# Kernel optimization log

Measured on AMD Instinct MI355X. Metric: run time of the kernel, lower is better.

Reference implementation:

```python
import jax, jax.numpy as jnp
import numpy as np

OFFSET = 1.0
BANDWIDTH = 0.5
EPS = 1e-5


def _similarity(source, target):
    # source: [b, c, h, w] -> [b, ns, c]; target: [b, c, h2, w2] -> [b, nt, c]
    b, c = source.shape[0], source.shape[1]
    s = source.reshape(b, c, -1).transpose(0, 2, 1)                  # [b, ns, c]
    t = target.reshape(b, target.shape[1], -1).transpose(0, 2, 1)    # [b, nt, c]
    s_sqr = jnp.sum(s * s, axis=-1)                                  # [b, ns]
    t_sqr = jnp.sum(t * t, axis=-1)                                  # [b, nt]
    # pairwise squared distances [b, nt, ns]
    dist = t_sqr[:, :, None] - 2.0 * jnp.einsum('btc,bsc->bts', t, s) + s_sqr[:, None, :]
    dist = jnp.maximum(dist, 0.0)
    # per source-column min over target rows (chunking in torch is per-column, hence equivalent globally)
    min_dist = jnp.min(dist, axis=1, keepdims=True)                  # [b, 1, ns]
    sim = jnp.exp((OFFSET - dist / (min_dist + EPS)) / BANDWIDTH)    # [b, nt, ns]
    sim = sim / jnp.sum(sim, axis=1, keepdims=True)                  # column-normalize over target dim
    # max over source columns per target row, then mean over target rows
    return jnp.mean(jnp.max(sim, axis=2), axis=-1)                   # [b]


def _loss(source, target):
    return jnp.mean(-jnp.log(_similarity(source, target)))


def setup_inputs() -> dict:
    key = jax.random.key(0)
    k1, k2 = jax.random.split(key)
    source = jax.random.normal(k1, (2, 128, 64, 64), dtype=jnp.float32)
    target = jax.random.normal(k2, (2, 128, 64, 64), dtype=jnp.float32)
    return {"source": source, "target": target}


def reference(source, target):
    # is_symmetric=True, is_similarity=False -> symmetric loss
    return (_loss(source, target) + _loss(target, source)) / 2.0
```

## Files before the change

kernel.cpp:

```cpp
#include <hip/hip_runtime.h>
#include <math.h>

#define NB 2
#define NC 128
#define NN 4096
#define C2L 2.88539008177792681472f

typedef __attribute__((ext_vector_type(8))) short short8;
typedef __attribute__((ext_vector_type(4))) float f32x4;

__device__ unsigned short g_Tb[NB][NN][NC];
__device__ unsigned short g_Sb[NB][NN][NC];
__device__ float g_tsqr[NB][NN];
__device__ float g_ssqr[NB][NN];
__device__ float g_rowS[NB][NN];
__device__ float g_rowLZ[NB][NN];
__device__ float g_rowE[NB][NN];
__device__ float g_colS[NB][NN];
__device__ float g_colLZ[NB][NN];
__device__ float g_colE[NB][NN];
__device__ float g_colpart[NB][128][NN];
__device__ float g_rowpart[NB][16][NN];

#if __has_builtin(__builtin_amdgcn_exp2f)
__device__ __forceinline__ float fexp2(float x) { return __builtin_amdgcn_exp2f(x); }
#else
__device__ __forceinline__ float fexp2(float x) { return exp2f(x); }
#endif

#define GLL16(gsrc, ldst) \
  __builtin_amdgcn_global_load_lds((const __attribute__((address_space(1))) void*)(gsrc), \
                                   (__attribute__((address_space(3))) void*)(ldst), 16, 0, 0)

__device__ __forceinline__ unsigned f2bf(float f) {
    unsigned u = __float_as_uint(f);
    u += 0x7FFFu + ((u >> 16) & 1u);
    return u >> 16;
}

__global__ void __launch_bounds__(256) transpose_prep(const float* __restrict__ src,
                                                      const float* __restrict__ tgt) {
    __shared__ float ls[NC][68];
    __shared__ float redn[4][64];
    int bid = blockIdx.x;
    int mat = bid >> 7;
    int b   = (bid >> 6) & 1;
    int n0  = (bid & 63) << 6;
    int tid = threadIdx.x;
    const float* in = (mat ? tgt : src) + (size_t)b * NC * NN;
    unsigned short (*out)[NC] = mat ? g_Tb[b] : g_Sb[b];
    float* sq = mat ? g_tsqr[b] : g_ssqr[b];

    for (int idx = tid; idx < NC * 16; idx += 256) {
        int k = idx >> 4, c4 = (idx & 15) << 2;
        *(float4*)&ls[k][c4] = *(const float4*)(in + (size_t)k * NN + n0 + c4);
    }
    __syncthreads();
    {
        int n = tid & 63, c = tid >> 6;
        float psum = 0.f;
        for (int cc = c; cc < 16; cc += 4) {
            unsigned uo[4];
            #pragma unroll
            for (int e = 0; e < 4; ++e) {
                float v0 = ls[cc * 8 + 2 * e][n];
                float v1 = ls[cc * 8 + 2 * e + 1][n];
                psum = fmaf(v0, v0, psum);
                psum = fmaf(v1, v1, psum);
                uo[e] = f2bf(v0) | (f2bf(v1) << 16);
            }
            int swz = mat ? cc : (cc ^ (n & 7));
            *(uint4*)&out[n0 + n][swz * 8] = make_uint4(uo[0], uo[1], uo[2], uo[3]);
        }
        redn[c][n] = psum;
    }
    __syncthreads();
    if (tid < 64)
        sq[n0 + tid] = (redn[0][tid] + redn[1][tid]) + (redn[2][tid] + redn[3][tid]);
}

template<int PASS>
__global__ void __launch_bounds__(256) sweep_kernel() {
    __shared__ unsigned short Sp[256 * NC];

    int bid = blockIdx.x;
    int b   = bid >> 9;
    int st  = (bid >> 4) & 31;
    int pn  = bid & 15;
    int i0  = st * 128;
    int j0  = pn * 256;
    int tid = threadIdx.x;
    int w = tid >> 6, lane = tid & 63, q = lane >> 4, x = lane & 15;
    int iw = i0 + w * 32;

    #pragma unroll
    for (int it = 0; it < 16; ++it) {
        int l = tid + it * 256;
        GLL16(&g_Sb[b][j0 + (l >> 4)][(l & 15) * 8], &Sp[l * 8]);
    }

    short8 af[2][4];
    #pragma unroll
    for (int m = 0; m < 2; ++m)
        #pragma unroll
        for (int kk = 0; kk < 4; ++kk)
            af[m][kk] = *(const short8*)&g_Tb[b][iw + m * 16 + x][(kk * 4 + q) * 8];

    float tq[8], rS[8], rC[8];
    #pragma unroll
    for (int m = 0; m < 2; ++m)
        #pragma unroll
        for (int v = 0; v < 4; ++v) {
            int row = iw + m * 16 + q * 4 + v;
            tq[m * 4 + v] = g_tsqr[b][row];
            rS[m * 4 + v] = (PASS >= 2) ? g_rowS[b][row] : 0.f;
            rC[m * 4 + v] = (PASS == 3) ? (C2L - g_rowLZ[b][row]) : 0.f;
        }

    float sqc[4], cSc[4], cCc[4], sqn[4], cSn[4], cCn[4];
    #pragma unroll
    for (int n = 0; n < 4; ++n) {
        int col = j0 + n * 16 + x;
        sqn[n] = g_ssqr[b][col];
        cSn[n] = (PASS >= 2) ? g_colS[b][col] : 0.f;
        cCn[n] = (PASS == 3) ? (C2L - g_colLZ[b][col]) : 0.f;
    }

    float rstate[8];
    #pragma unroll
    for (int e = 0; e < 8; ++e)
        rstate[e] = (PASS == 1) ? 3.0e38f : (PASS == 2 ? 0.f : -3.0e38f);

    __syncthreads();

    for (int jt = 0; jt < 4; ++jt) {
        #pragma unroll
        for (int n = 0; n < 4; ++n) { sqc[n] = sqn[n]; cSc[n] = cSn[n]; cCc[n] = cCn[n]; }
        if (jt < 3) {
            #pragma unroll
            for (int n = 0; n < 4; ++n) {
                int col = j0 + (jt + 1) * 64 + n * 16 + x;
                sqn[n] = g_ssqr[b][col];
                if (PASS >= 2) cSn[n] = g_colS[b][col];
                if (PASS == 3) cCn[n] = C2L - g_colLZ[b][col];
            }
        }

        f32x4 acc[2][4];
        #pragma unroll
        for (int m = 0; m < 2; ++m)
            #pragma unroll
            for (int n = 0; n < 4; ++n)
                acc[m][n] = (f32x4){0.f, 0.f, 0.f, 0.f};

        #pragma unroll
        for (int kk = 0; kk < 4; ++kk) {
            short8 bf[4];
            #pragma unroll
            for (int n = 0; n < 4; ++n) {
                int r  = jt * 64 + n * 16 + x;
                int ch = (kk * 4 + q) ^ (r & 7);
                bf[n] = *(const short8*)&Sp[r * NC + ch * 8];
            }
            #pragma unroll
            for (int m = 0; m < 2; ++m)
                #pragma unroll
                for (int n = 0; n < 4; ++n)
                    acc[m][n] = __builtin_amdgcn_mfma_f32_16x16x32_bf16(af[m][kk], bf[n], acc[m][n], 0, 0, 0);
        }

        float cstate[4];
        #pragma unroll
        for (int n = 0; n < 4; ++n)
            cstate[n] = (PASS == 1) ? 3.0e38f : (PASS == 2 ? 0.f : -3.0e38f);

        #pragma unroll
        for (int m = 0; m < 2; ++m)
            #pragma unroll
            for (int n = 0; n < 4; ++n)
                #pragma unroll
                for (int v = 0; v < 4; ++v) {
                    float dv = fmaxf(fmaf(-2.f, acc[m][n][v], tq[m * 4 + v] + sqc[n]), 0.f);
                    if (PASS == 1) {
                        rstate[m * 4 + v] = fminf(rstate[m * 4 + v], dv);
                        cstate[n]         = fminf(cstate[n], dv);
                    } else if (PASS == 2) {
                        rstate[m * 4 + v] += fexp2(fmaf(dv, rS[m * 4 + v], C2L));
                        cstate[n]         += fexp2(fmaf(dv, cSc[n], C2L));
                    } else {
                        rstate[m * 4 + v] = fmaxf(rstate[m * 4 + v], fmaf(dv, cSc[n], cCc[n]));
                        cstate[n]         = fmaxf(cstate[n], fmaf(dv, rS[m * 4 + v], rC[m * 4 + v]));
                    }
                }

        #pragma unroll
        for (int off = 16; off < 64; off <<= 1)
            #pragma unroll
            for (int n = 0; n < 4; ++n) {
                float o = __shfl_xor(cstate[n], off);
                cstate[n] = (PASS == 1) ? fminf(cstate[n], o)
                           : (PASS == 2) ? cstate[n] + o : fmaxf(cstate[n], o);
            }
        if (q == 0)
            #pragma unroll
            for (int n = 0; n < 4; ++n)
                g_colpart[b][st * 4 + w][j0 + jt * 64 + n * 16 + x] = cstate[n];
    }

    #pragma unroll
    for (int off = 1; off < 16; off <<= 1)
        #pragma unroll
        for (int e = 0; e < 8; ++e) {
            float o = __shfl_xor(rstate[e], off);
            rstate[e] = (PASS == 1) ? fminf(rstate[e], o)
                       : (PASS == 2) ? rstate[e] + o : fmaxf(rstate[e], o);
        }
    if (x == 0)
        #pragma unroll
        for (int e = 0; e < 8; ++e)
            g_rowpart[b][pn][iw + (e >> 2) * 16 + q * 4 + (e & 3)] = rstate[e];
}

template<int PASS>
__global__ void __launch_bounds__(256) reduce_kernel() {
    int bid = blockIdx.x;
    int b = bid >> 6, g = bid & 63;
    int tid = threadIdx.x;
    int el = g * 64 + (tid >> 2);
    int part = tid & 3;

    float ca = (PASS == 1) ? 3.0e38f : (PASS == 2 ? 0.f : -3.0e38f);
    float ra = ca;
    #pragma unroll 4
    for (int s = part * 32; s < part * 32 + 32; ++s) {
        float cv = g_colpart[b][s][el];
        if (PASS == 1) ca = fminf(ca, cv);
        else if (PASS == 2) ca += cv;
        else ca = fmaxf(ca, cv);
    }
    #pragma unroll
    for (int s = part * 4; s < part * 4 + 4; ++s) {
        float rv = g_rowpart[b][s][el];
        if (PASS == 1) ra = fminf(ra, rv);
        else if (PASS == 2) ra += rv;
        else ra = fmaxf(ra, rv);
    }
    #pragma unroll
    for (int off = 1; off < 4; off <<= 1) {
        float co = __shfl_xor(ca, off), ro = __shfl_xor(ra, off);
        if (PASS == 1) { ca = fminf(ca, co); ra = fminf(ra, ro); }
        else if (PASS == 2) { ca += co; ra += ro; }
        else { ca = fmaxf(ca, co); ra = fmaxf(ra, ro); }
    }
    if (part == 0) {
        if (PASS == 1) { g_colS[b][el] = -(C2L / (ca + 1e-5f)); g_rowS[b][el] = -(C2L / (ra + 1e-5f)); }
        if (PASS == 2) { g_colLZ[b][el] = log2f(ca);            g_rowLZ[b][el] = log2f(ra); }
        if (PASS == 3) { g_colE[b][el] = fexp2(ca);             g_rowE[b][el] = fexp2(ra); }
    }
}

__global__ void final_kernel(float* __restrict__ out) {
    int tid = threadIdx.x;
    float s[4] = {0.f, 0.f, 0.f, 0.f};
    for (int i = tid; i < NN; i += 256) {
        s[0] += g_rowE[0][i];
        s[1] += g_rowE[1][i];
        s[2] += g_colE[0][i];
        s[3] += g_colE[1][i];
    }
    __shared__ float red[4][4];
    int lane = tid & 63, w = tid >> 6;
    #pragma unroll
    for (int t = 0; t < 4; ++t) {
        float v = s[t];
        #pragma unroll
        for (int off = 32; off; off >>= 1) v += __shfl_down(v, off);
        if (lane == 0) red[t][w] = v;
    }
    __syncthreads();
    if (tid == 0) {
        float o = 0.f;
        #pragma unroll
        for (int t = 0; t < 4; ++t) {
            float S = red[t][0] + red[t][1] + red[t][2] + red[t][3];
            o += logf(S);
        }
        out[0] = logf((float)NN) - 0.25f * o;
    }
}

extern "C" void kernel_launch(void* const* d_in, const int* in_sizes, int n_in,
                              void* d_out, int out_size, void* d_ws, size_t ws_size,
                              hipStream_t stream) {
    const float* src = (const float*)d_in[0];
    const float* tgt = (const float*)d_in[1];
    (void)in_sizes; (void)n_in; (void)d_ws; (void)ws_size; (void)out_size;

    transpose_prep<<<256, 256, 0, stream>>>(src, tgt);
    sweep_kernel<1><<<1024, 256, 0, stream>>>();
    reduce_kernel<1><<<128, 256, 0, stream>>>();
    sweep_kernel<2><<<1024, 256, 0, stream>>>();
    reduce_kernel<2><<<128, 256, 0, stream>>>();
    sweep_kernel<3><<<1024, 256, 0, stream>>>();
    reduce_kernel<3><<<128, 256, 0, stream>>>();
    final_kernel<<<1, 256, 0, stream>>>((float*)d_out);
}
```

Before: 99.25 us.

## Quantize operands to FP8 e4m3 and use FP8 MFMA for distance GEMM

Inputs are now converted to FP8 (e4m3) instead of bf16 in the prep kernel, and the squared norms are computed from the dequantized values so they stay consistent with the dot products. The sweep kernels use the fp8 16x16x32 MFMA with 8-byte operand fragments, and the shared-memory staging and swizzle are rebuilt for byte-sized elements. This halves global and LDS traffic for the operand tiles and shrinks the LDS footprint per block. The cost is a large loss of precision in the pairwise distances, which feed a ratio and an exponential, so the loss may deviate noticeably from the reference.

```diff
diff --git a/kernel.cpp b/kernel.cpp
--- a/kernel.cpp
+++ b/kernel.cpp
@@ -6,11 +6,10 @@
 #define NN 4096
 #define C2L 2.88539008177792681472f
 
-typedef __attribute__((ext_vector_type(8))) short short8;
 typedef __attribute__((ext_vector_type(4))) float f32x4;
 
-__device__ unsigned short g_Tb[NB][NN][NC];
-__device__ unsigned short g_Sb[NB][NN][NC];
+__device__ __align__(16) unsigned char g_Tb[NB][NN][NC];
+__device__ __align__(16) unsigned char g_Sb[NB][NN][NC];
 __device__ float g_tsqr[NB][NN];
 __device__ float g_ssqr[NB][NN];
 __device__ float g_rowS[NB][NN];
@@ -32,10 +31,25 @@
   __builtin_amdgcn_global_load_lds((const __attribute__((address_space(1))) void*)(gsrc), \
                                    (__attribute__((address_space(3))) void*)(ldst), 16, 0, 0)
 
-__device__ __forceinline__ unsigned f2bf(float f) {
+__device__ __forceinline__ unsigned f2fp8_1(float f) {
     unsigned u = __float_as_uint(f);
-    u += 0x7FFFu + ((u >> 16) & 1u);
-    return u >> 16;
+    unsigned s = (u >> 31) << 7;
+    float a = fabsf(f);
+    if (!(a >= 0.015625f)) return s;
+    if (a > 448.f) return s | 0x7E;
+    unsigned au = u & 0x7FFFFFFFu;
+    unsigned r  = au + 0x7FFFFu + ((au >> 20) & 1u);
+    int e4 = (int)(r >> 23) - 127 + 7;
+    unsigned m = (r >> 20) & 7u;
+    if (e4 > 15 || (e4 == 15 && m == 7)) return s | 0x7E;
+    if (e4 <= 0) return s;
+    return s | ((unsigned)e4 << 3) | m;
+}
+__device__ __forceinline__ float up8(unsigned w, int sel) {
+    unsigned b = (w >> (sel * 8)) & 0xFF;
+    unsigned s = b >> 7, e = (b >> 3) & 15, m = b & 7;
+    if (e == 0) { float v = (float)m * 0.001953125f; return s ? -v : v; }
+    return __uint_as_float((s << 31) | ((e + 120) << 23) | (m << 20));
 }
 
 __global__ void __launch_bounds__(256) transpose_prep(const float* __restrict__ src,
@@ -48,7 +62,7 @@
     int n0  = (bid & 63) << 6;
     int tid = threadIdx.x;
     const float* in = (mat ? tgt : src) + (size_t)b * NC * NN;
-    unsigned short (*out)[NC] = mat ? g_Tb[b] : g_Sb[b];
+    unsigned char (*out)[NC] = mat ? g_Tb[b] : g_Sb[b];
     float* sq = mat ? g_tsqr[b] : g_ssqr[b];
 
     for (int idx = tid; idx < NC * 16; idx += 256) {
@@ -59,18 +73,23 @@
     {
         int n = tid & 63, c = tid >> 6;
         float psum = 0.f;
-        for (int cc = c; cc < 16; cc += 4) {
+        for (int cc = c; cc < 8; cc += 4) {
             unsigned uo[4];
             #pragma unroll
             for (int e = 0; e < 4; ++e) {
-                float v0 = ls[cc * 8 + 2 * e][n];
-                float v1 = ls[cc * 8 + 2 * e + 1][n];
-                psum = fmaf(v0, v0, psum);
-                psum = fmaf(v1, v1, psum);
-                uo[e] = f2bf(v0) | (f2bf(v1) << 16);
+                unsigned wv = 0;
+                #pragma unroll
+                for (int j = 0; j < 4; ++j) {
+                    float v = ls[cc * 16 + e * 4 + j][n];
+                    unsigned p = f2fp8_1(v);
+                    wv |= p << (j * 8);
+                    float rv = up8(p, 0);
+                    psum = fmaf(rv, rv, psum);
+                }
+                uo[e] = wv;
             }
             int swz = mat ? cc : (cc ^ (n & 7));
-            *(uint4*)&out[n0 + n][swz * 8] = make_uint4(uo[0], uo[1], uo[2], uo[3]);
+            *(uint4*)&out[n0 + n][swz * 16] = make_uint4(uo[0], uo[1], uo[2], uo[3]);
         }
         redn[c][n] = psum;
     }
@@ -81,7 +100,7 @@
 
 template<int PASS>
 __global__ void __launch_bounds__(256) sweep_kernel() {
-    __shared__ unsigned short Sp[256 * NC];
+    __shared__ __align__(16) unsigned char Sp[256 * NC];
 
     int bid = blockIdx.x;
     int b   = bid >> 9;
@@ -94,17 +113,17 @@
     int iw = i0 + w * 32;
 
     #pragma unroll
-    for (int it = 0; it < 16; ++it) {
+    for (int it = 0; it < 8; ++it) {
         int l = tid + it * 256;
-        GLL16(&g_Sb[b][j0 + (l >> 4)][(l & 15) * 8], &Sp[l * 8]);
-    }
-
-    short8 af[2][4];
+        GLL16(&g_Sb[b][j0 + (l >> 3)][(l & 7) * 16], &Sp[l * 16]);
+    }
+
+    long af[2][4];
     #pragma unroll
     for (int m = 0; m < 2; ++m)
         #pragma unroll
         for (int kk = 0; kk < 4; ++kk)
-            af[m][kk] = *(const short8*)&g_Tb[b][iw + m * 16 + x][(kk * 4 + q) * 8];
+            af[m][kk] = *(const long*)&g_Tb[b][iw + m * 16 + x][(kk * 4 + q) * 8];
 
     float tq[8], rS[8], rC[8];
     #pragma unroll
@@ -155,18 +174,19 @@
 
         #pragma unroll
         for (int kk = 0; kk < 4; ++kk) {
-            short8 bf[4];
+            long bf[4];
             #pragma unroll
             for (int n = 0; n < 4; ++n) {
                 int r  = jt * 64 + n * 16 + x;
-                int ch = (kk * 4 + q) ^ (r & 7);
-                bf[n] = *(const short8*)&Sp[r * NC + ch * 8];
+                int k0 = (kk * 4 + q) * 8;
+                int ad = r * NC + (((k0 >> 4) ^ (r & 7)) << 4) + (k0 & 8);
+                bf[n] = *(const long*)&Sp[ad];
             }
             #pragma unroll
             for (int m = 0; m < 2; ++m)
                 #pragma unroll
                 for (int n = 0; n < 4; ++n)
-                    acc[m][n] = __builtin_amdgcn_mfma_f32_16x16x32_bf16(af[m][kk], bf[n], acc[m][n], 0, 0, 0);
+                    acc[m][n] = __builtin_amdgcn_mfma_f32_16x16x32_fp8_fp8(af[m][kk], bf[n], acc[m][n], 0, 0, 0);
         }
 
         float cstate[4];
```

After: 105.2 us. 5.9% more time.
